# Performance work log

Hardware: AMD Instinct MI355X
Metric: run time of the kernel (lower is better)

The kernel has to match this reference:

```python
import jax, jax.numpy as jnp
import numpy as np

# Module config (matches init_kwargs)
IC, OC, K, R, C, STRIDE = 128, 256, 3, 64, 64, 1
TAPS = 576
B = 16
BIAS_LEN = 128
H_OUT = (R - K) // STRIDE + 1  # 62
W_OUT = (C - K) // STRIDE + 1  # 62


def setup_inputs() -> dict:
    key = jax.random.key(0)
    k1, k2, k3 = jax.random.split(key, 3)
    rng = np.random.default_rng(0)
    # Per output channel, choose TAPS distinct (c, ky, kx) taps out of IC*K*K.
    all_taps = IC * K * K
    tap_ids = np.stack([rng.choice(all_taps, TAPS, replace=False) for _ in range(OC)])  # [OC, TAPS]
    c = tap_ids // (K * K)
    rem = tap_ids % (K * K)
    ky, kx = rem // K, rem % K
    # Flattened gather index into a [IC, R, C] image, exactly as the CUDA module builds it.
    image_weight_index = (c * (R * C) + ky * C + kx).astype(np.int32).reshape(-1)  # [OC*TAPS]
    filter_lengths = np.full(OC, TAPS, dtype=np.int32)
    start_points = (np.arange(OC, dtype=np.int64) * TAPS).astype(np.int32)
    bias_index = rng.choice(OC, BIAS_LEN, replace=False).astype(np.int32)
    return {
        "images": jax.random.normal(k1, (B, IC, R, C), jnp.float32),
        "weight_value": jax.random.normal(k2, (OC * TAPS,), jnp.float32) * 0.05,
        "image_weight_index": jnp.asarray(image_weight_index),
        "filter_lengths": jnp.asarray(filter_lengths),
        "start_points": jnp.asarray(start_points),
        "bias_index": jnp.asarray(bias_index),
        "bias_value": jax.random.normal(k3, (BIAS_LEN,), jnp.float32),
    }


def reference(images, weight_value, image_weight_index, filter_lengths, start_points, bias_index, bias_value):
    nnz = weight_value.shape[0]
    # Taps are stored contiguously per output channel (start_points = cumsum of filter_lengths).
    oc_ids = jnp.repeat(jnp.arange(OC), filter_lengths, total_repeat_length=nnz)
    # Decode flattened image index back to (in_channel, ky, kx).
    c = image_weight_index // (R * C)
    rem = image_weight_index % (R * C)
    ky, kx = rem // C, rem % C
    # Scatter sparse taps into a dense OIHW kernel; the gather-conv math is then
    # an exact VALID strided cross-correlation.
    W = jnp.zeros((OC, IC, K, K), images.dtype).at[oc_ids, c, ky, kx].add(weight_value)
    out = jax.lax.conv_general_dilated(
        images, W, window_strides=(STRIDE, STRIDE), padding="VALID",
        dimension_numbers=("NCHW", "OIHW", "NCHW"))  # [B, OC, H_OUT, W_OUT]
    # Conditional bias: channel oc gets bias_value[j] for each j with bias_index[j] == oc.
    bias = jnp.zeros((OC,), images.dtype).at[bias_index].add(bias_value)
    return out + bias[None, :, None, None]
```

## Files before the change

### kernel.cpp

```cpp
#include <hip/hip_runtime.h>
#include <stdint.h>

#define IC 128
#define OC 256
#define RR 64
#define CCOLS 64
#define HO 62
#define WO 62
#define NB 16

#define W9T_BYTES (9 * OC * IC * 2)
#define W9T_PAD   131072
#define CHUNK_STRIDE 8192
#define LDS_TOTAL 102400

typedef __bf16 bf16x8 __attribute__((ext_vector_type(8)));
typedef float f32x16 __attribute__((ext_vector_type(16)));

__device__ __forceinline__ unsigned short f2bf(float f) {
    unsigned u = __builtin_bit_cast(unsigned, f);
    u += 0x7FFFu + ((u >> 16) & 1u);
    return (unsigned short)(u >> 16);
}

__global__ void prep_weights(const float* __restrict__ wv,
                             const int* __restrict__ iwi,
                             const int* __restrict__ flen,
                             const int* __restrict__ sp,
                             unsigned char* __restrict__ W9Tf,
                             const int* __restrict__ bias_index,
                             const float* __restrict__ bias_value,
                             float* __restrict__ bias_dense, int nbias) {
    if (blockIdx.x == OC) {
        int t = threadIdx.x;
        if (t < OC) bias_dense[t] = 0.f;
        __syncthreads();
        if (t < nbias) atomicAdd(&bias_dense[bias_index[t]], bias_value[t]);
        return;
    }
    const int oc = blockIdx.x;
    const int s = sp[oc];
    const int n = flen[oc];
    const int g = oc >> 5;
    for (int t = threadIdx.x; t < n; t += blockDim.x) {
        const int ix = iwi[s + t];
        const int c = ix >> 12;
        const int rem = ix & 4095;
        const int ky = rem >> 6, kx = rem & 63;
        const int kp = ky * 3 + kx;
        const int ck = c >> 4;
        const int khalf = (c >> 3) & 1;
        const int lane = (oc & 31) + (khalf << 5);
        const size_t off = (size_t)(kp * 8 + ck) * CHUNK_STRIDE +
                           g * 1024 + lane * 16 + (c & 7) * 2;
        *(unsigned short*)(W9Tf + off) = f2bf(wv[s + t]);
    }
}

#define KSTEP_L(CK, AV0, AV1, C00, C01, C10, C11, N00, N01, N10, N11, PB0, PB1, POFF) \
  {                                                                           \
    asm volatile("ds_read_b128 %0, %1 offset:%c2" : "=v"(N00) : "v"(PB0), "i"(POFF)); \
    asm volatile("ds_read_b128 %0, %1 offset:%c2" : "=v"(N01) : "v"(PB1), "i"((POFF) + 512)); \
    asm volatile("ds_read_b128 %0, %1 offset:%c2" : "=v"(N10) : "v"(PB0), "i"((POFF) + 16384)); \
    asm volatile("ds_read_b128 %0, %1 offset:%c2" : "=v"(N11) : "v"(PB1), "i"((POFF) + 16896)); \
    asm volatile("s_waitcnt vmcnt(6) lgkmcnt(4)"                              \
                 : "+v"(AV0), "+v"(AV1), "+v"(C00), "+v"(C01), "+v"(C10), "+v"(C11)); \
    c000 = __builtin_amdgcn_mfma_f32_32x32x16_bf16(AV0, C00, c000, 0, 0, 0);  \
    c100 = __builtin_amdgcn_mfma_f32_32x32x16_bf16(AV1, C00, c100, 0, 0, 0);  \
    c001 = __builtin_amdgcn_mfma_f32_32x32x16_bf16(AV0, C01, c001, 0, 0, 0);  \
    c101 = __builtin_amdgcn_mfma_f32_32x32x16_bf16(AV1, C01, c101, 0, 0, 0);  \
    c010 = __builtin_amdgcn_mfma_f32_32x32x16_bf16(AV0, C10, c010, 0, 0, 0);  \
    c110 = __builtin_amdgcn_mfma_f32_32x32x16_bf16(AV1, C10, c110, 0, 0, 0);  \
    c011 = __builtin_amdgcn_mfma_f32_32x32x16_bf16(AV0, C11, c011, 0, 0, 0);  \
    c111 = __builtin_amdgcn_mfma_f32_32x32x16_bf16(AV1, C11, c111, 0, 0, 0);  \
    asm volatile("global_load_dwordx4 %0, %1, %2" : "=v"(AV0)                 \
                 : "v"(vA0), "s"((const void*)(pWg + ((CK) + 4) * CHUNK_STRIDE))); \
    asm volatile("global_load_dwordx4 %0, %1, %2" : "=v"(AV1)                 \
                 : "v"(vA1), "s"((const void*)(pWg + ((CK) + 4) * CHUNK_STRIDE))); \
  }

__global__ __launch_bounds__(512, 2) void conv_mfma(
    const float* __restrict__ images,
    const unsigned char* __restrict__ W9Tf,
    const float* __restrict__ bias_dense,
    float* __restrict__ out)
{
    int y0 = blockIdx.x * 4;
    if (y0 > 58) y0 = 58;
    const int b = blockIdx.y;
    const int t = threadIdx.x;
    const int w = t >> 6;
    const int wq = w & 3;
    const int ypg = w >> 2;
    const int l = t & 63;
    const int lm = l & 31;
    const int lhi = l >> 5;

    __shared__ unsigned char lds[LDS_TOTAL];

    const float* __restrict__ imgb = images + (size_t)b * (IC * RR * CCOLS);

    {
        const int xs = t & 63;
        const int og = t >> 6;
        #pragma unroll
        for (int krow = 0; krow < 6; ++krow) {
            #pragma unroll
            for (int h = 0; h < 2; ++h) {
                const int o = og + 8 * h;
                const int c0 = o * 8;
                const float* __restrict__ p =
                    imgb + (size_t)c0 * (RR * CCOLS) + (y0 + krow) * CCOLS + xs;
                unsigned v0, v1, v2, v3;
                v0 = (unsigned)f2bf(p[0])              | ((unsigned)f2bf(p[RR * CCOLS])     << 16);
                v1 = (unsigned)f2bf(p[2 * RR * CCOLS]) | ((unsigned)f2bf(p[3 * RR * CCOLS]) << 16);
                v2 = (unsigned)f2bf(p[4 * RR * CCOLS]) | ((unsigned)f2bf(p[5 * RR * CCOLS]) << 16);
                v3 = (unsigned)f2bf(p[6 * RR * CCOLS]) | ((unsigned)f2bf(p[7 * RR * CCOLS]) << 16);
                *(uint4*)(lds + krow * 16384 + o * 1024 + xs * 16) =
                    make_uint4(v0, v1, v2, v3);
            }
        }
    }

    const int vA0 = (2 * wq + 0) * 1024 + l * 16;
    const int vA1 = (2 * wq + 1) * 1024 + l * 16;
    const int lmc = lm > 29 ? 29 : lm;
    const unsigned bB0 = (unsigned)(uintptr_t)(lds + ypg * 32768 + lhi * 1024 + lm * 16);
    const unsigned bB1 = (unsigned)(uintptr_t)(lds + ypg * 32768 + lhi * 1024 + lmc * 16);

    __syncthreads();

    const unsigned char* pWg = W9Tf;
    bf16x8 a0S0, a0S1, a0S2, a0S3, a1S0, a1S1, a1S2, a1S3;
    bf16x8 bX00, bX01, bX10, bX11, bY00, bY01, bY10, bY11;
    asm volatile("global_load_dwordx4 %0, %1, %2" : "=v"(a0S0) : "v"(vA0), "s"((const void*)(pWg)));
    asm volatile("global_load_dwordx4 %0, %1, %2" : "=v"(a1S0) : "v"(vA1), "s"((const void*)(pWg)));
    asm volatile("global_load_dwordx4 %0, %1, %2" : "=v"(a0S1) : "v"(vA0), "s"((const void*)(pWg + CHUNK_STRIDE)));
    asm volatile("global_load_dwordx4 %0, %1, %2" : "=v"(a1S1) : "v"(vA1), "s"((const void*)(pWg + CHUNK_STRIDE)));
    asm volatile("global_load_dwordx4 %0, %1, %2" : "=v"(a0S2) : "v"(vA0), "s"((const void*)(pWg + 2 * CHUNK_STRIDE)));
    asm volatile("global_load_dwordx4 %0, %1, %2" : "=v"(a1S2) : "v"(vA1), "s"((const void*)(pWg + 2 * CHUNK_STRIDE)));
    asm volatile("global_load_dwordx4 %0, %1, %2" : "=v"(a0S3) : "v"(vA0), "s"((const void*)(pWg + 3 * CHUNK_STRIDE)));
    asm volatile("global_load_dwordx4 %0, %1, %2" : "=v"(a1S3) : "v"(vA1), "s"((const void*)(pWg + 3 * CHUNK_STRIDE)));
    asm volatile("ds_read_b128 %0, %1" : "=v"(bX00) : "v"(bB0));
    asm volatile("ds_read_b128 %0, %1 offset:512" : "=v"(bX01) : "v"(bB1));
    asm volatile("ds_read_b128 %0, %1 offset:16384" : "=v"(bX10) : "v"(bB0));
    asm volatile("ds_read_b128 %0, %1 offset:16896" : "=v"(bX11) : "v"(bB1));

    f32x16 c000 = {}, c001 = {}, c010 = {}, c011 = {};
    f32x16 c100 = {}, c101 = {}, c110 = {}, c111 = {};

    unsigned vB0c = bB0, vB1c = bB1;
    #pragma clang loop unroll(disable)
    for (int g = 0; g < 9; ++g) {
        const unsigned delta = ((0x124u >> g) & 1u) ? 16352u : 16u;
        const unsigned vB0n = vB0c + delta;
        const unsigned vB1n = vB1c + delta;
        KSTEP_L(0, a0S0, a1S0, bX00, bX01, bX10, bX11, bY00, bY01, bY10, bY11, vB0c, vB1c, 1 * 2048)
        KSTEP_L(1, a0S1, a1S1, bY00, bY01, bY10, bY11, bX00, bX01, bX10, bX11, vB0c, vB1c, 2 * 2048)
        KSTEP_L(2, a0S2, a1S2, bX00, bX01, bX10, bX11, bY00, bY01, bY10, bY11, vB0c, vB1c, 3 * 2048)
        KSTEP_L(3, a0S3, a1S3, bY00, bY01, bY10, bY11, bX00, bX01, bX10, bX11, vB0c, vB1c, 4 * 2048)
        KSTEP_L(4, a0S0, a1S0, bX00, bX01, bX10, bX11, bY00, bY01, bY10, bY11, vB0c, vB1c, 5 * 2048)
        KSTEP_L(5, a0S1, a1S1, bY00, bY01, bY10, bY11, bX00, bX01, bX10, bX11, vB0c, vB1c, 6 * 2048)
        KSTEP_L(6, a0S2, a1S2, bX00, bX01, bX10, bX11, bY00, bY01, bY10, bY11, vB0c, vB1c, 7 * 2048)
        KSTEP_L(7, a0S3, a1S3, bY00, bY01, bY10, bY11, bX00, bX01, bX10, bX11, vB0n, vB1n, 0)
        vB0c = vB0n; vB1c = vB1n;
        pWg += 8 * CHUNK_STRIDE;
    }

    asm volatile("s_waitcnt vmcnt(0) lgkmcnt(0)"
                 : "+v"(a0S0), "+v"(a0S1), "+v"(a0S2), "+v"(a0S3),
                   "+v"(a1S0), "+v"(a1S1), "+v"(a1S2), "+v"(a1S3),
                   "+v"(bX00), "+v"(bX01), "+v"(bX10), "+v"(bX11),
                   "+v"(bY00), "+v"(bY01), "+v"(bY10), "+v"(bY11));

    const int yb = y0 + 2 * ypg;
    #pragma unroll
    for (int m = 0; m < 2; ++m) {
        const int ocw = (2 * wq + m) * 32;
        const f32x16 d00 = m ? c100 : c000;
        const f32x16 d01 = m ? c101 : c001;
        const f32x16 d10 = m ? c110 : c010;
        const f32x16 d11 = m ? c111 : c011;
        #pragma unroll
        for (int r = 0; r < 16; ++r) {
            const int oc = ocw + (r & 3) + 8 * (r >> 2) + 4 * lhi;
            const float bv = bias_dense[oc];
            const size_t ob0 = (((size_t)b * OC + oc) * HO + yb) * WO;
            out[ob0 + lm] = d00[r] + bv;
            if (lm < 30)
                out[ob0 + 32 + lm] = d01[r] + bv;
            const size_t ob1 = ob0 + WO;
            out[ob1 + lm] = d10[r] + bv;
            if (lm < 30)
                out[ob1 + 32 + lm] = d11[r] + bv;
        }
    }
}

extern "C" void kernel_launch(void* const* d_in, const int* in_sizes, int n_in,
                              void* d_out, int out_size, void* d_ws, size_t ws_size,
                              hipStream_t stream) {
    const float* images             = (const float*)d_in[0];
    const float* weight_value       = (const float*)d_in[1];
    const int*   image_weight_index = (const int*)d_in[2];
    const int*   filter_lengths     = (const int*)d_in[3];
    const int*   start_points       = (const int*)d_in[4];
    const int*   bias_index         = (const int*)d_in[5];
    const float* bias_value         = (const float*)d_in[6];
    float* out = (float*)d_out;

    unsigned char* W9Tf = (unsigned char*)d_ws;
    float* bias_dense = (float*)((char*)d_ws + W9T_BYTES + W9T_PAD);

    hipMemsetAsync(d_ws, 0, W9T_BYTES + W9T_PAD, stream);
    prep_weights<<<OC + 1, 256, 0, stream>>>(weight_value, image_weight_index,
                                             filter_lengths, start_points, W9Tf,
                                             bias_index, bias_value, bias_dense,
                                             in_sizes[5]);

    dim3 grid(16, NB);
    conv_mfma<<<grid, 512, 0, stream>>>(images, W9Tf, bias_dense, out);
}
```

Baseline: 56.47 us.

## Double block size so each wave computes one output row

Blocks now launch 1024 threads (16 waves) instead of 512. Each wave handles a single output row rather than two, so it keeps half the accumulators and LDS reads per k-step. The weight prefetch depth drops from 4 to 2 chunks to save registers. The aim is more waves per block for latency hiding and lower register pressure. The cost is that each wave now loads the weights for only one row, so weight global loads per output double, and the shallower prefetch may expose more memory latency.

New measurement: 63.78 us. 12.9% more time.

```diff
diff --git a/kernel.cpp b/kernel.cpp
--- a/kernel.cpp
+++ b/kernel.cpp
@@ -57,29 +57,23 @@
     }
 }
 
-#define KSTEP_L(CK, AV0, AV1, C00, C01, C10, C11, N00, N01, N10, N11, PB0, PB1, POFF) \
+#define KSTEP_L(CK, AV0, AV1, C0, C1, N0, N1, PB0, PB1, POFF)                 \
   {                                                                           \
-    asm volatile("ds_read_b128 %0, %1 offset:%c2" : "=v"(N00) : "v"(PB0), "i"(POFF)); \
-    asm volatile("ds_read_b128 %0, %1 offset:%c2" : "=v"(N01) : "v"(PB1), "i"((POFF) + 512)); \
-    asm volatile("ds_read_b128 %0, %1 offset:%c2" : "=v"(N10) : "v"(PB0), "i"((POFF) + 16384)); \
-    asm volatile("ds_read_b128 %0, %1 offset:%c2" : "=v"(N11) : "v"(PB1), "i"((POFF) + 16896)); \
-    asm volatile("s_waitcnt vmcnt(6) lgkmcnt(4)"                              \
-                 : "+v"(AV0), "+v"(AV1), "+v"(C00), "+v"(C01), "+v"(C10), "+v"(C11)); \
-    c000 = __builtin_amdgcn_mfma_f32_32x32x16_bf16(AV0, C00, c000, 0, 0, 0);  \
-    c100 = __builtin_amdgcn_mfma_f32_32x32x16_bf16(AV1, C00, c100, 0, 0, 0);  \
-    c001 = __builtin_amdgcn_mfma_f32_32x32x16_bf16(AV0, C01, c001, 0, 0, 0);  \
-    c101 = __builtin_amdgcn_mfma_f32_32x32x16_bf16(AV1, C01, c101, 0, 0, 0);  \
-    c010 = __builtin_amdgcn_mfma_f32_32x32x16_bf16(AV0, C10, c010, 0, 0, 0);  \
-    c110 = __builtin_amdgcn_mfma_f32_32x32x16_bf16(AV1, C10, c110, 0, 0, 0);  \
-    c011 = __builtin_amdgcn_mfma_f32_32x32x16_bf16(AV0, C11, c011, 0, 0, 0);  \
-    c111 = __builtin_amdgcn_mfma_f32_32x32x16_bf16(AV1, C11, c111, 0, 0, 0);  \
+    asm volatile("ds_read_b128 %0, %1 offset:%c2" : "=v"(N0) : "v"(PB0), "i"(POFF)); \
+    asm volatile("ds_read_b128 %0, %1 offset:%c2" : "=v"(N1) : "v"(PB1), "i"((POFF) + 512)); \
+    asm volatile("s_waitcnt vmcnt(2) lgkmcnt(2)"                              \
+                 : "+v"(AV0), "+v"(AV1), "+v"(C0), "+v"(C1));                 \
+    c00 = __builtin_amdgcn_mfma_f32_32x32x16_bf16(AV0, C0, c00, 0, 0, 0);     \
+    c10 = __builtin_amdgcn_mfma_f32_32x32x16_bf16(AV1, C0, c10, 0, 0, 0);     \
+    c01 = __builtin_amdgcn_mfma_f32_32x32x16_bf16(AV0, C1, c01, 0, 0, 0);     \
+    c11 = __builtin_amdgcn_mfma_f32_32x32x16_bf16(AV1, C1, c11, 0, 0, 0);     \
     asm volatile("global_load_dwordx4 %0, %1, %2" : "=v"(AV0)                 \
-                 : "v"(vA0), "s"((const void*)(pWg + ((CK) + 4) * CHUNK_STRIDE))); \
+                 : "v"(vA0), "s"((const void*)(pWg + ((CK) + 2) * CHUNK_STRIDE))); \
     asm volatile("global_load_dwordx4 %0, %1, %2" : "=v"(AV1)                 \
-                 : "v"(vA1), "s"((const void*)(pWg + ((CK) + 4) * CHUNK_STRIDE))); \
+                 : "v"(vA1), "s"((const void*)(pWg + ((CK) + 2) * CHUNK_STRIDE))); \
   }
 
-__global__ __launch_bounds__(512, 2) void conv_mfma(
+__global__ __launch_bounds__(1024, 1) void conv_mfma(
     const float* __restrict__ images,
     const unsigned char* __restrict__ W9Tf,
     const float* __restrict__ bias_dense,
@@ -91,7 +85,7 @@
     const int t = threadIdx.x;
     const int w = t >> 6;
     const int wq = w & 3;
-    const int ypg = w >> 2;
+    const int yr = w >> 2;
     const int l = t & 63;
     const int lm = l & 31;
     const int lhi = l >> 5;
@@ -102,52 +96,41 @@
 
     {
         const int xs = t & 63;
-        const int og = t >> 6;
+        const int o = t >> 6;
+        const int c0 = o * 8;
         #pragma unroll
         for (int krow = 0; krow < 6; ++krow) {
-            #pragma unroll
-            for (int h = 0; h < 2; ++h) {
-                const int o = og + 8 * h;
-                const int c0 = o * 8;
-                const float* __restrict__ p =
-                    imgb + (size_t)c0 * (RR * CCOLS) + (y0 + krow) * CCOLS + xs;
-                unsigned v0, v1, v2, v3;
-                v0 = (unsigned)f2bf(p[0])              | ((unsigned)f2bf(p[RR * CCOLS])     << 16);
-                v1 = (unsigned)f2bf(p[2 * RR * CCOLS]) | ((unsigned)f2bf(p[3 * RR * CCOLS]) << 16);
-                v2 = (unsigned)f2bf(p[4 * RR * CCOLS]) | ((unsigned)f2bf(p[5 * RR * CCOLS]) << 16);
-                v3 = (unsigned)f2bf(p[6 * RR * CCOLS]) | ((unsigned)f2bf(p[7 * RR * CCOLS]) << 16);
-                *(uint4*)(lds + krow * 16384 + o * 1024 + xs * 16) =
-                    make_uint4(v0, v1, v2, v3);
-            }
+            const float* __restrict__ p =
+                imgb + (size_t)c0 * (RR * CCOLS) + (y0 + krow) * CCOLS + xs;
+            unsigned v0, v1, v2, v3;
+            v0 = (unsigned)f2bf(p[0])              | ((unsigned)f2bf(p[RR * CCOLS])     << 16);
+            v1 = (unsigned)f2bf(p[2 * RR * CCOLS]) | ((unsigned)f2bf(p[3 * RR * CCOLS]) << 16);
+            v2 = (unsigned)f2bf(p[4 * RR * CCOLS]) | ((unsigned)f2bf(p[5 * RR * CCOLS]) << 16);
+            v3 = (unsigned)f2bf(p[6 * RR * CCOLS]) | ((unsigned)f2bf(p[7 * RR * CCOLS]) << 16);
+            *(uint4*)(lds + krow * 16384 + o * 1024 + xs * 16) =
+                make_uint4(v0, v1, v2, v3);
         }
     }
 
     const int vA0 = (2 * wq + 0) * 1024 + l * 16;
     const int vA1 = (2 * wq + 1) * 1024 + l * 16;
     const int lmc = lm > 29 ? 29 : lm;
-    const unsigned bB0 = (unsigned)(uintptr_t)(lds + ypg * 32768 + lhi * 1024 + lm * 16);
-    const unsigned bB1 = (unsigned)(uintptr_t)(lds + ypg * 32768 + lhi * 1024 + lmc * 16);
+    const unsigned bB0 = (unsigned)(uintptr_t)(lds + yr * 16384 + lhi * 1024 + lm * 16);
+    const unsigned bB1 = (unsigned)(uintptr_t)(lds + yr * 16384 + lhi * 1024 + lmc * 16);
 
     __syncthreads();
 
     const unsigned char* pWg = W9Tf;
-    bf16x8 a0S0, a0S1, a0S2, a0S3, a1S0, a1S1, a1S2, a1S3;
-    bf16x8 bX00, bX01, bX10, bX11, bY00, bY01, bY10, bY11;
+    bf16x8 a0S0, a0S1, a1S0, a1S1;
+    bf16x8 bX0, bX1, bY0, bY1;
     asm volatile("global_load_dwordx4 %0, %1, %2" : "=v"(a0S0) : "v"(vA0), "s"((const void*)(pWg)));
     asm volatile("global_load_dwordx4 %0, %1, %2" : "=v"(a1S0) : "v"(vA1), "s"((const void*)(pWg)));
     asm volatile("global_load_dwordx4 %0, %1, %2" : "=v"(a0S1) : "v"(vA0), "s"((const void*)(pWg + CHUNK_STRIDE)));
     asm volatile("global_load_dwordx4 %0, %1, %2" : "=v"(a1S1) : "v"(vA1), "s"((const void*)(pWg + CHUNK_STRIDE)));
-    asm volatile("global_load_dwordx4 %0, %1, %2" : "=v"(a0S2) : "v"(vA0), "s"((const void*)(pWg + 2 * CHUNK_STRIDE)));
-    asm volatile("global_load_dwordx4 %0, %1, %2" : "=v"(a1S2) : "v"(vA1), "s"((const void*)(pWg + 2 * CHUNK_STRIDE)));
-    asm volatile("global_load_dwordx4 %0, %1, %2" : "=v"(a0S3) : "v"(vA0), "s"((const void*)(pWg + 3 * CHUNK_STRIDE)));
-    asm volatile("global_load_dwordx4 %0, %1, %2" : "=v"(a1S3) : "v"(vA1), "s"((const void*)(pWg + 3 * CHUNK_STRIDE)));
-    asm volatile("ds_read_b128 %0, %1" : "=v"(bX00) : "v"(bB0));
-    asm volatile("ds_read_b128 %0, %1 offset:512" : "=v"(bX01) : "v"(bB1));
-    asm volatile("ds_read_b128 %0, %1 offset:16384" : "=v"(bX10) : "v"(bB0));
-    asm volatile("ds_read_b128 %0, %1 offset:16896" : "=v"(bX11) : "v"(bB1));
+    asm volatile("ds_read_b128 %0, %1" : "=v"(bX0) : "v"(bB0));
+    asm volatile("ds_read_b128 %0, %1 offset:512" : "=v"(bX1) : "v"(bB1));
 
-    f32x16 c000 = {}, c001 = {}, c010 = {}, c011 = {};
-    f32x16 c100 = {}, c101 = {}, c110 = {}, c111 = {};
+    f32x16 c00 = {}, c01 = {}, c10 = {}, c11 = {};
 
     unsigned vB0c = bB0, vB1c = bB1;
     #pragma clang loop unroll(disable)
@@ -155,44 +138,36 @@
         const unsigned delta = ((0x124u >> g) & 1u) ? 16352u : 16u;
         const unsigned vB0n = vB0c + delta;
         const unsigned vB1n = vB1c + delta;
-        KSTEP_L(0, a0S0, a1S0, bX00, bX01, bX10, bX11, bY00, bY01, bY10, bY11, vB0c, vB1c, 1 * 2048)
-        KSTEP_L(1, a0S1, a1S1, bY00, bY01, bY10, bY11, bX00, bX01, bX10, bX11, vB0c, vB1c, 2 * 2048)
-        KSTEP_L(2, a0S2, a1S2, bX00, bX01, bX10, bX11, bY00, bY01, bY10, bY11, vB0c, vB1c, 3 * 2048)
-        KSTEP_L(3, a0S3, a1S3, bY00, bY01, bY10, bY11, bX00, bX01, bX10, bX11, vB0c, vB1c, 4 * 2048)
-        KSTEP_L(4, a0S0, a1S0, bX00, bX01, bX10, bX11, bY00, bY01, bY10, bY11, vB0c, vB1c, 5 * 2048)
-        KSTEP_L(5, a0S1, a1S1, bY00, bY01, bY10, bY11, bX00, bX01, bX10, bX11, vB0c, vB1c, 6 * 2048)
-        KSTEP_L(6, a0S2, a1S2, bX00, bX01, bX10, bX11, bY00, bY01, bY10, bY11, vB0c, vB1c, 7 * 2048)
-        KSTEP_L(7, a0S3, a1S3, bY00, bY01, bY10, bY11, bX00, bX01, bX10, bX11, vB0n, vB1n, 0)
+        KSTEP_L(0, a0S0, a1S0, bX0, bX1, bY0, bY1, vB0c, vB1c, 1 * 2048)
+        KSTEP_L(1, a0S1, a1S1, bY0, bY1, bX0, bX1, vB0c, vB1c, 2 * 2048)
+        KSTEP_L(2, a0S0, a1S0, bX0, bX1, bY0, bY1, vB0c, vB1c, 3 * 2048)
+        KSTEP_L(3, a0S1, a1S1, bY0, bY1, bX0, bX1, vB0c, vB1c, 4 * 2048)
+        KSTEP_L(4, a0S0, a1S0, bX0, bX1, bY0, bY1, vB0c, vB1c, 5 * 2048)
+        KSTEP_L(5, a0S1, a1S1, bY0, bY1, bX0, bX1, vB0c, vB1c, 6 * 2048)
+        KSTEP_L(6, a0S0, a1S0, bX0, bX1, bY0, bY1, vB0c, vB1c, 7 * 2048)
+        KSTEP_L(7, a0S1, a1S1, bY0, bY1, bX0, bX1, vB0n, vB1n, 0)
         vB0c = vB0n; vB1c = vB1n;
         pWg += 8 * CHUNK_STRIDE;
     }
 
     asm volatile("s_waitcnt vmcnt(0) lgkmcnt(0)"
-                 : "+v"(a0S0), "+v"(a0S1), "+v"(a0S2), "+v"(a0S3),
-                   "+v"(a1S0), "+v"(a1S1), "+v"(a1S2), "+v"(a1S3),
-                   "+v"(bX00), "+v"(bX01), "+v"(bX10), "+v"(bX11),
-                   "+v"(bY00), "+v"(bY01), "+v"(bY10), "+v"(bY11));
+                 : "+v"(a0S0), "+v"(a0S1), "+v"(a1S0), "+v"(a1S1),
+                   "+v"(bX0), "+v"(bX1), "+v"(bY0), "+v"(bY1));
 
-    const int yb = y0 + 2 * ypg;
+    const int yb = y0 + yr;
     #pragma unroll
     for (int m = 0; m < 2; ++m) {
         const int ocw = (2 * wq + m) * 32;
-        const f32x16 d00 = m ? c100 : c000;
-        const f32x16 d01 = m ? c101 : c001;
-        const f32x16 d10 = m ? c110 : c010;
-        const f32x16 d11 = m ? c111 : c011;
+        const f32x16 d0 = m ? c10 : c00;
+        const f32x16 d1 = m ? c11 : c01;
         #pragma unroll
         for (int r = 0; r < 16; ++r) {
             const int oc = ocw + (r & 3) + 8 * (r >> 2) + 4 * lhi;
             const float bv = bias_dense[oc];
-            const size_t ob0 = (((size_t)b * OC + oc) * HO + yb) * WO;
-            out[ob0 + lm] = d00[r] + bv;
+            const size_t ob = (((size_t)b * OC + oc) * HO + yb) * WO;
+            out[ob + lm] = d0[r] + bv;
             if (lm < 30)
-                out[ob0 + 32 + lm] = d01[r] + bv;
-            const size_t ob1 = ob0 + WO;
-            out[ob1 + lm] = d10[r] + bv;
-            if (lm < 30)
-                out[ob1 + 32 + lm] = d11[r] + bv;
+                out[ob + 32 + lm] = d1[r] + bv;
         }
     }
 }
@@ -219,5 +194,5 @@
                                              in_sizes[5]);
 
     dim3 grid(16, NB);
-    conv_mfma<<<grid, 512, 0, stream>>>(images, W9Tf, bias_dense, out);
+    conv_mfma<<<grid, 1024, 0, stream>>>(images, W9Tf, bias_dense, out);
 }
```
